# Performance work log

Hardware: AMD Instinct MI355X
Metric: run time of the kernel (lower is better)

The kernel has to match this reference:

```python
import jax, jax.numpy as jnp
import numpy as np

B, N, D = 32, 1024, 512

def setup_inputs() -> dict:
    key = jax.random.key(0)
    ks = jax.random.split(key, 5)
    s = 1.0 / np.sqrt(D)
    return {
        "x": jax.random.normal(ks[0], (B, N, D), jnp.float32),
        "Wq": jax.random.normal(ks[1], (D, D), jnp.float32) * s,
        "bq": jnp.zeros((D,), jnp.float32),
        "Wk": jax.random.normal(ks[2], (D, D), jnp.float32) * s,
        "bk": jnp.zeros((D,), jnp.float32),
        "Wv": jax.random.normal(ks[3], (D, D), jnp.float32) * s,
        "bv": jnp.zeros((D,), jnp.float32),
        "pos_bias": jax.random.normal(ks[4], (N, N), jnp.float32) * 0.02,
    }

def reference(x, Wq, bq, Wk, bk, Wv, bv, pos_bias):
    # torch nn.Linear: y = x @ W.T + b
    q = x @ Wq.T + bq                      # [B,N,D]
    k = x @ Wk.T + bk                      # [B,N,D]
    v = x @ Wv.T + bv                      # [B,N,D]
    # AFT-full: out[b,t,d] = sig(q)[b,t,d] * sum_s exp(k[b,s,d]+w[t,s]) v[b,s,d]
    #                                        / sum_s exp(k[b,s,d]+w[t,s])
    # exp(k+w) factors as exp(w)*exp(k); the num/den ratio is invariant to
    # per-row shifts of w and per-(b,d) shifts of k, so stabilize both.
    w = pos_bias - jnp.max(pos_bias, axis=1, keepdims=True)   # [T,S]
    kk = k - jnp.max(k, axis=1, keepdims=True)                # [B,S,D]
    ew = jnp.exp(w)
    ek = jnp.exp(kk)
    num = jnp.einsum('ts,bsd->btd', ew, ek * v)               # [B,T,D]
    den = jnp.einsum('ts,bsd->btd', ew, ek)                   # [B,T,D]
    return jax.nn.sigmoid(q) * (num / den)
```

## Files before the change

### kernel.cpp

```cpp
#include <hip/hip_runtime.h>

typedef unsigned short u16;
typedef unsigned int u32;
using frag8 = __attribute__((ext_vector_type(8))) short;
using f32x4 = __attribute__((ext_vector_type(4))) float;

__device__ __forceinline__ u16 f2bf(float f) {
  union { float f; u32 u; } x;
  x.f = f;
  u32 r = (x.u + 0x7fffu + ((x.u >> 16) & 1u)) >> 16;
  return (u16)r;
}

__device__ __forceinline__ void stage_tile64(const u16* g, int ld, u16* lds, int tid) {
  const int wv = tid >> 6;
#pragma unroll
  for (int i = 0; i < 4; ++i) {
    const int c = i * 256 + tid;
    const int row = c >> 3;
    const int colc = (c & 7) ^ (row & 7);
    __builtin_amdgcn_global_load_lds(
        (const __attribute__((address_space(1))) void*)(g + (size_t)row * ld + colc * 8),
        (__attribute__((address_space(3))) void*)(lds + (size_t)(i * 256 + wv * 64) * 8),
        16, 0, 0);
  }
}

__device__ __forceinline__ frag8 frag_read64(const u16* lds, int row, int kk, int quad) {
  const int cc = (kk * 4 + quad) ^ (row & 7);
  return *(const frag8*)&lds[row * 64 + cc * 8];
}

__global__ void prep_kernel(const float* __restrict__ x, const float* __restrict__ Wq,
                            const float* __restrict__ Wk, const float* __restrict__ Wv,
                            const float* __restrict__ pb, u16* __restrict__ xb,
                            u16* __restrict__ wqb, u16* __restrict__ wkb,
                            u16* __restrict__ wvb, u16* __restrict__ ewb) {
  const int blk = blockIdx.x;
  const float* src;
  u16* dst;
  int base;
  bool ex = false;
  if (blk < 4096)      { src = x;  dst = xb;  base = blk; }
  else if (blk < 4160) { src = Wq; dst = wqb; base = blk - 4096; }
  else if (blk < 4224) { src = Wk; dst = wkb; base = blk - 4160; }
  else if (blk < 4288) { src = Wv; dst = wvb; base = blk - 4224; }
  else                 { src = pb; dst = ewb; base = blk - 4288; ex = true; }
#pragma unroll
  for (int j = 0; j < 4; ++j) {
    const int i = base * 1024 + j * 256 + threadIdx.x;
    float4 v = ((const float4*)src)[i];
    ushort4 o;
    if (ex) {
      o.x = f2bf(__expf(v.x)); o.y = f2bf(__expf(v.y));
      o.z = f2bf(__expf(v.z)); o.w = f2bf(__expf(v.w));
    } else {
      o.x = f2bf(v.x); o.y = f2bf(v.y); o.z = f2bf(v.z); o.w = f2bf(v.w);
    }
    ((ushort4*)dst)[i] = o;
  }
}

__global__ __launch_bounds__(256, 2) void qkv_kernel(const u16* __restrict__ xb,
                                                     const u16* __restrict__ wqb,
                                                     const u16* __restrict__ wkb,
                                                     const u16* __restrict__ wvb,
                                                     const float* __restrict__ bq,
                                                     const float* __restrict__ bk,
                                                     const float* __restrict__ bv,
                                                     float* __restrict__ out,
                                                     u16* __restrict__ ekT,
                                                     u16* __restrict__ ekvT) {
  __shared__ __align__(16) u16 sh[3 * 128 * 64];
  const int tid = threadIdx.x;
  const int lane = tid & 63, wv = tid >> 6;
  const int wm = (wv & 1) * 64, wn = (wv >> 1) * 64;
  const int fr = lane & 15, quad = lane >> 4;
  const int bid = blockIdx.x;

  if ((bid & 1) == 0) {
    const int qb = bid >> 1;
    const int n0 = (qb & 3) * 128;
    const int m0 = (qb >> 2) * 128;
    u16* As = sh;
    u16* Bs = sh + 8192;
    f32x4 acc[4][4] = {};
    for (int k0 = 0; k0 < 512; k0 += 64) {
      stage_tile64(xb + (size_t)m0 * 512 + k0, 512, As, tid);
      stage_tile64(wqb + (size_t)n0 * 512 + k0, 512, Bs, tid);
      __syncthreads();
#pragma unroll
      for (int kk = 0; kk < 2; ++kk) {
        frag8 a[4], b[4];
#pragma unroll
        for (int i = 0; i < 4; ++i) {
          a[i] = frag_read64(As, wm + i * 16 + fr, kk, quad);
          b[i] = frag_read64(Bs, wn + i * 16 + fr, kk, quad);
        }
#pragma unroll
        for (int mi = 0; mi < 4; ++mi)
#pragma unroll
          for (int ni = 0; ni < 4; ++ni)
            acc[mi][ni] = __builtin_amdgcn_mfma_f32_16x16x32_bf16(a[mi], b[ni], acc[mi][ni], 0, 0, 0);
      }
      __syncthreads();
    }
#pragma unroll
    for (int mi = 0; mi < 4; ++mi)
#pragma unroll
      for (int ni = 0; ni < 4; ++ni) {
        const int col = n0 + wn + ni * 16 + fr;
        const float bqv = bq[col];
#pragma unroll
        for (int r = 0; r < 4; ++r) {
          const int row = m0 + wm + mi * 16 + quad * 4 + r;
          const float qv = acc[mi][ni][r] + bqv;
          out[(size_t)row * 512 + col] = 1.0f / (1.0f + __expf(-qv));
        }
      }
  } else {
    const int kvb = bid >> 1;
    const int s0 = (kvb & 7) * 128;
    const int d0 = ((kvb >> 3) & 3) * 128;
    const int b  = kvb >> 5;
    u16* Ak = sh;
    u16* Av = sh + 8192;
    u16* Bs = sh + 16384;
    f32x4 acck[4][4] = {}, accv[4][4] = {};
    for (int k0 = 0; k0 < 512; k0 += 64) {
      stage_tile64(wkb + (size_t)d0 * 512 + k0, 512, Ak, tid);
      stage_tile64(wvb + (size_t)d0 * 512 + k0, 512, Av, tid);
      stage_tile64(xb + ((size_t)b * 1024 + s0) * 512 + k0, 512, Bs, tid);
      __syncthreads();
#pragma unroll
      for (int kk = 0; kk < 2; ++kk) {
        frag8 ak[4], av[4], bb[4];
#pragma unroll
        for (int i = 0; i < 4; ++i) {
          ak[i] = frag_read64(Ak, wm + i * 16 + fr, kk, quad);
          av[i] = frag_read64(Av, wm + i * 16 + fr, kk, quad);
          bb[i] = frag_read64(Bs, wn + i * 16 + fr, kk, quad);
        }
#pragma unroll
        for (int mi = 0; mi < 4; ++mi)
#pragma unroll
          for (int ni = 0; ni < 4; ++ni) {
            acck[mi][ni] = __builtin_amdgcn_mfma_f32_16x16x32_bf16(ak[mi], bb[ni], acck[mi][ni], 0, 0, 0);
            accv[mi][ni] = __builtin_amdgcn_mfma_f32_16x16x32_bf16(av[mi], bb[ni], accv[mi][ni], 0, 0, 0);
          }
      }
      __syncthreads();
    }
#pragma unroll
    for (int mi = 0; mi < 4; ++mi)
#pragma unroll
      for (int r = 0; r < 4; ++r) {
        const int d = d0 + wm + mi * 16 + quad * 4 + r;
        const float bkv = bk[d], bvv = bv[d];
#pragma unroll
        for (int ni = 0; ni < 4; ++ni) {
          const int s = s0 + wn + ni * 16 + fr;
          const float ek = __expf(acck[mi][ni][r] + bkv);
          const float vv = accv[mi][ni][r] + bvv;
          const size_t idx = ((size_t)b * 512 + d) * 1024 + s;
          ekT[idx]  = f2bf(ek);
          ekvT[idx] = f2bf(ek * vv);
        }
      }
  }
}

__global__ __launch_bounds__(256, 2) void aft_kernel(const u16* __restrict__ ew,
                                                     const u16* __restrict__ ekT,
                                                     const u16* __restrict__ ekvT,
                                                     float* __restrict__ out) {
  __shared__ __align__(16) u16 As[128 * 64];
  __shared__ __align__(16) u16 B1[128 * 64];
  __shared__ __align__(16) u16 B2[128 * 64];
  const int tid = threadIdx.x;
  const int lane = tid & 63, wv = tid >> 6;
  const int wm = (wv & 1) * 64, wn = (wv >> 1) * 64;
  const int fr = lane & 15, quad = lane >> 4;
  const int d0 = blockIdx.x * 128;
  const int t0 = blockIdx.y * 128;
  const int b  = blockIdx.z;
  f32x4 accn[4][4] = {}, accd[4][4] = {};
  for (int k0 = 0; k0 < 1024; k0 += 64) {
    stage_tile64(ew + (size_t)t0 * 1024 + k0, 1024, As, tid);
    stage_tile64(ekvT + ((size_t)b * 512 + d0) * 1024 + k0, 1024, B1, tid);
    stage_tile64(ekT + ((size_t)b * 512 + d0) * 1024 + k0, 1024, B2, tid);
    __syncthreads();
#pragma unroll
    for (int kk = 0; kk < 2; ++kk) {
      frag8 a[4], b1[4], b2[4];
#pragma unroll
      for (int i = 0; i < 4; ++i) {
        a[i]  = frag_read64(As, wm + i * 16 + fr, kk, quad);
        b1[i] = frag_read64(B1, wn + i * 16 + fr, kk, quad);
        b2[i] = frag_read64(B2, wn + i * 16 + fr, kk, quad);
      }
#pragma unroll
      for (int mi = 0; mi < 4; ++mi)
#pragma unroll
        for (int ni = 0; ni < 4; ++ni) {
          accn[mi][ni] = __builtin_amdgcn_mfma_f32_16x16x32_bf16(a[mi], b1[ni], accn[mi][ni], 0, 0, 0);
          accd[mi][ni] = __builtin_amdgcn_mfma_f32_16x16x32_bf16(a[mi], b2[ni], accd[mi][ni], 0, 0, 0);
        }
    }
    __syncthreads();
  }
#pragma unroll
  for (int mi = 0; mi < 4; ++mi)
#pragma unroll
    for (int ni = 0; ni < 4; ++ni)
#pragma unroll
      for (int r = 0; r < 4; ++r) {
        const int t = t0 + wm + mi * 16 + quad * 4 + r;
        const int d = d0 + wn + ni * 16 + fr;
        const size_t idx = ((size_t)b * 1024 + t) * 512 + d;
        const float sq = out[idx];
        out[idx] = sq * accn[mi][ni][r] / accd[mi][ni][r];
      }
}

extern "C" void kernel_launch(void* const* d_in, const int* in_sizes, int n_in,
                              void* d_out, int out_size, void* d_ws, size_t ws_size,
                              hipStream_t stream) {
  const float* x  = (const float*)d_in[0];
  const float* Wq = (const float*)d_in[1];
  const float* bq = (const float*)d_in[2];
  const float* Wk = (const float*)d_in[3];
  const float* bk = (const float*)d_in[4];
  const float* Wv = (const float*)d_in[5];
  const float* bv = (const float*)d_in[6];
  const float* pb = (const float*)d_in[7];
  float* out = (float*)d_out;
  char* ws = (char*)d_ws;
  u16* xb   = (u16*)(ws);
  u16* wqb  = (u16*)(ws + 33554432);
  u16* wkb  = (u16*)(ws + 34078720);
  u16* wvb  = (u16*)(ws + 34603008);
  u16* ewb  = (u16*)(ws + 35127296);
  u16* ekT  = (u16*)(ws + 37224448);
  u16* ekvT = (u16*)(ws + 70778880);

  prep_kernel<<<4544, 256, 0, stream>>>(x, Wq, Wk, Wv, pb, xb, wqb, wkb, wvb, ewb);
  qkv_kernel<<<2048, 256, 0, stream>>>(xb, wqb, wkb, wvb, bq, bk, bv, out, ekT, ekvT);
  aft_kernel<<<dim3(4, 8, 32), 256, 0, stream>>>(ewb, ekT, ekvT, out);
}
```

Before: 267.8 us.

## Fuse Q, K, V projections into one block sharing the staged x tile

The separate Q blocks and K/V blocks are merged into a single kernel in which each block stages one x tile plus the Wq, Wk and Wv tiles and computes all three projections. K and V use a swapped MFMA operand order, so their output is transposed to directly feed the ekT/ekvT layout. This stages each x tile once instead of twice and halves the grid, at the cost of 48 accumulator fragments per thread and more shared memory. The added register pressure may cut occupancy or cause spills.

```diff
diff --git a/kernel.cpp b/kernel.cpp
--- a/kernel.cpp
+++ b/kernel.cpp
@@ -61,113 +61,96 @@
   }
 }
 
-__global__ __launch_bounds__(256, 2) void qkv_kernel(const u16* __restrict__ xb,
-                                                     const u16* __restrict__ wqb,
-                                                     const u16* __restrict__ wkb,
-                                                     const u16* __restrict__ wvb,
-                                                     const float* __restrict__ bq,
-                                                     const float* __restrict__ bk,
-                                                     const float* __restrict__ bv,
-                                                     float* __restrict__ out,
-                                                     u16* __restrict__ ekT,
-                                                     u16* __restrict__ ekvT) {
-  __shared__ __align__(16) u16 sh[3 * 128 * 64];
+__global__ __launch_bounds__(256, 2) void qkvu_kernel(const u16* __restrict__ xb,
+                                                      const u16* __restrict__ wqb,
+                                                      const u16* __restrict__ wkb,
+                                                      const u16* __restrict__ wvb,
+                                                      const float* __restrict__ bq,
+                                                      const float* __restrict__ bk,
+                                                      const float* __restrict__ bv,
+                                                      float* __restrict__ out,
+                                                      u16* __restrict__ ekT,
+                                                      u16* __restrict__ ekvT) {
+  __shared__ __align__(16) u16 Xs[128 * 64];
+  __shared__ __align__(16) u16 Ws_q[128 * 64];
+  __shared__ __align__(16) u16 Ws_k[128 * 64];
+  __shared__ __align__(16) u16 Ws_v[128 * 64];
   const int tid = threadIdx.x;
   const int lane = tid & 63, wv = tid >> 6;
-  const int wm = (wv & 1) * 64, wn = (wv >> 1) * 64;
+  const int wmx = (wv & 1) * 64;
+  const int wnw = (wv >> 1) * 64;
   const int fr = lane & 15, quad = lane >> 4;
-  const int bid = blockIdx.x;
-
-  if ((bid & 1) == 0) {
-    const int qb = bid >> 1;
-    const int n0 = (qb & 3) * 128;
-    const int m0 = (qb >> 2) * 128;
-    u16* As = sh;
-    u16* Bs = sh + 8192;
-    f32x4 acc[4][4] = {};
-    for (int k0 = 0; k0 < 512; k0 += 64) {
-      stage_tile64(xb + (size_t)m0 * 512 + k0, 512, As, tid);
-      stage_tile64(wqb + (size_t)n0 * 512 + k0, 512, Bs, tid);
-      __syncthreads();
-#pragma unroll
-      for (int kk = 0; kk < 2; ++kk) {
-        frag8 a[4], b[4];
-#pragma unroll
-        for (int i = 0; i < 4; ++i) {
-          a[i] = frag_read64(As, wm + i * 16 + fr, kk, quad);
-          b[i] = frag_read64(Bs, wn + i * 16 + fr, kk, quad);
-        }
+  const int n0 = (blockIdx.x & 3) * 128;
+  const int mt = blockIdx.x >> 2;
+  const int m0 = mt * 128;
+  const int b  = mt >> 3;
+  const int s0 = (mt & 7) * 128;
+
+  f32x4 accq[4][4] = {}, acck[4][4] = {}, accv[4][4] = {};
+  for (int k0 = 0; k0 < 512; k0 += 64) {
+    stage_tile64(xb + (size_t)m0 * 512 + k0, 512, Xs, tid);
+    stage_tile64(wqb + (size_t)n0 * 512 + k0, 512, Ws_q, tid);
+    stage_tile64(wkb + (size_t)n0 * 512 + k0, 512, Ws_k, tid);
+    stage_tile64(wvb + (size_t)n0 * 512 + k0, 512, Ws_v, tid);
+    __syncthreads();
+#pragma unroll
+    for (int kk = 0; kk < 2; ++kk) {
+      frag8 xa[4], wb[4];
+#pragma unroll
+      for (int i = 0; i < 4; ++i) xa[i] = frag_read64(Xs, wmx + i * 16 + fr, kk, quad);
+#pragma unroll
+      for (int i = 0; i < 4; ++i) wb[i] = frag_read64(Ws_q, wnw + i * 16 + fr, kk, quad);
+#pragma unroll
+      for (int mi = 0; mi < 4; ++mi)
+#pragma unroll
+        for (int ni = 0; ni < 4; ++ni)
+          accq[mi][ni] = __builtin_amdgcn_mfma_f32_16x16x32_bf16(xa[mi], wb[ni], accq[mi][ni], 0, 0, 0);
+#pragma unroll
+      for (int i = 0; i < 4; ++i) wb[i] = frag_read64(Ws_k, wnw + i * 16 + fr, kk, quad);
+#pragma unroll
+      for (int ni = 0; ni < 4; ++ni)
 #pragma unroll
         for (int mi = 0; mi < 4; ++mi)
-#pragma unroll
-          for (int ni = 0; ni < 4; ++ni)
-            acc[mi][ni] = __builtin_amdgcn_mfma_f32_16x16x32_bf16(a[mi], b[ni], acc[mi][ni], 0, 0, 0);
-      }
-      __syncthreads();
-    }
-#pragma unroll
-    for (int mi = 0; mi < 4; ++mi)
-#pragma unroll
-      for (int ni = 0; ni < 4; ++ni) {
-        const int col = n0 + wn + ni * 16 + fr;
-        const float bqv = bq[col];
-#pragma unroll
-        for (int r = 0; r < 4; ++r) {
-          const int row = m0 + wm + mi * 16 + quad * 4 + r;
-          const float qv = acc[mi][ni][r] + bqv;
-          out[(size_t)row * 512 + col] = 1.0f / (1.0f + __expf(-qv));
-        }
-      }
-  } else {
-    const int kvb = bid >> 1;
-    const int s0 = (kvb & 7) * 128;
-    const int d0 = ((kvb >> 3) & 3) * 128;
-    const int b  = kvb >> 5;
-    u16* Ak = sh;
-    u16* Av = sh + 8192;
-    u16* Bs = sh + 16384;
-    f32x4 acck[4][4] = {}, accv[4][4] = {};
-    for (int k0 = 0; k0 < 512; k0 += 64) {
-      stage_tile64(wkb + (size_t)d0 * 512 + k0, 512, Ak, tid);
-      stage_tile64(wvb + (size_t)d0 * 512 + k0, 512, Av, tid);
-      stage_tile64(xb + ((size_t)b * 1024 + s0) * 512 + k0, 512, Bs, tid);
-      __syncthreads();
-#pragma unroll
-      for (int kk = 0; kk < 2; ++kk) {
-        frag8 ak[4], av[4], bb[4];
-#pragma unroll
-        for (int i = 0; i < 4; ++i) {
-          ak[i] = frag_read64(Ak, wm + i * 16 + fr, kk, quad);
-          av[i] = frag_read64(Av, wm + i * 16 + fr, kk, quad);
-          bb[i] = frag_read64(Bs, wn + i * 16 + fr, kk, quad);
-        }
+          acck[ni][mi] = __builtin_amdgcn_mfma_f32_16x16x32_bf16(wb[ni], xa[mi], acck[ni][mi], 0, 0, 0);
+#pragma unroll
+      for (int i = 0; i < 4; ++i) wb[i] = frag_read64(Ws_v, wnw + i * 16 + fr, kk, quad);
+#pragma unroll
+      for (int ni = 0; ni < 4; ++ni)
 #pragma unroll
         for (int mi = 0; mi < 4; ++mi)
-#pragma unroll
-          for (int ni = 0; ni < 4; ++ni) {
-            acck[mi][ni] = __builtin_amdgcn_mfma_f32_16x16x32_bf16(ak[mi], bb[ni], acck[mi][ni], 0, 0, 0);
-            accv[mi][ni] = __builtin_amdgcn_mfma_f32_16x16x32_bf16(av[mi], bb[ni], accv[mi][ni], 0, 0, 0);
-          }
-      }
-      __syncthreads();
-    }
-#pragma unroll
-    for (int mi = 0; mi < 4; ++mi)
+          accv[ni][mi] = __builtin_amdgcn_mfma_f32_16x16x32_bf16(wb[ni], xa[mi], accv[ni][mi], 0, 0, 0);
+    }
+    __syncthreads();
+  }
+#pragma unroll
+  for (int mi = 0; mi < 4; ++mi)
+#pragma unroll
+    for (int ni = 0; ni < 4; ++ni) {
+      const int col = n0 + wnw + ni * 16 + fr;
+      const float bqv = bq[col];
 #pragma unroll
       for (int r = 0; r < 4; ++r) {
-        const int d = d0 + wm + mi * 16 + quad * 4 + r;
-        const float bkv = bk[d], bvv = bv[d];
-#pragma unroll
-        for (int ni = 0; ni < 4; ++ni) {
-          const int s = s0 + wn + ni * 16 + fr;
-          const float ek = __expf(acck[mi][ni][r] + bkv);
-          const float vv = accv[mi][ni][r] + bvv;
-          const size_t idx = ((size_t)b * 512 + d) * 1024 + s;
-          ekT[idx]  = f2bf(ek);
-          ekvT[idx] = f2bf(ek * vv);
-        }
-      }
-  }
+        const int row = m0 + wmx + mi * 16 + quad * 4 + r;
+        const float qv = accq[mi][ni][r] + bqv;
+        out[(size_t)row * 512 + col] = 1.0f / (1.0f + __expf(-qv));
+      }
+    }
+#pragma unroll
+  for (int ni = 0; ni < 4; ++ni)
+#pragma unroll
+    for (int r = 0; r < 4; ++r) {
+      const int d = n0 + wnw + ni * 16 + quad * 4 + r;
+      const float bkv = bk[d], bvv = bv[d];
+#pragma unroll
+      for (int mi = 0; mi < 4; ++mi) {
+        const int s = s0 + wmx + mi * 16 + fr;
+        const float ek = __expf(acck[ni][mi][r] + bkv);
+        const float vvv = accv[ni][mi][r] + bvv;
+        const size_t idx = ((size_t)b * 512 + d) * 1024 + s;
+        ekT[idx]  = f2bf(ek);
+        ekvT[idx] = f2bf(ek * vvv);
+      }
+    }
 }
 
 __global__ __launch_bounds__(256, 2) void aft_kernel(const u16* __restrict__ ew,
@@ -245,6 +228,6 @@
   u16* ekvT = (u16*)(ws + 70778880);
 
   prep_kernel<<<4544, 256, 0, stream>>>(x, Wq, Wk, Wv, pb, xb, wqb, wkb, wvb, ewb);
-  qkv_kernel<<<2048, 256, 0, stream>>>(xb, wqb, wkb, wvb, bq, bk, bv, out, ekT, ekvT);
+  qkvu_kernel<<<1024, 256, 0, stream>>>(xb, wqb, wkb, wvb, bq, bk, bv, out, ekT, ekvT);
   aft_kernel<<<dim3(4, 8, 32), 256, 0, stream>>>(ewb, ekT, ekvT, out);
 }
```

Result: faster. 258.4 us (median of 2 runs) (-3.5%).
